# Optimization experiments

Measured on AMD Instinct MI355X. Metric: run time of the kernel, lower is better.

The kernel has to match this reference:

```python
import jax, jax.numpy as jnp
import numpy as np

B, T, V, H, E, F, NM = 128, 32, 10000, 512, 512, 2048, 512
D0 = E + NM + H   # 1536: layer-0 concat(x, h)
D1 = H + H        # 1024: layer-1 concat(h_prev_layer, h)


def setup_inputs() -> dict:
    key = jax.random.key(0)
    ks = jax.random.split(key, 10)
    cnn_features = jax.random.normal(ks[0], (B, F), jnp.float32)
    x_tokens = jax.random.randint(ks[1], (B, T), 0, V)
    current_hidden_state = jnp.zeros((2, B, 2 * H), jnp.float32)
    embedding = jax.random.normal(ks[2], (V, E), jnp.float32)
    W_in = jax.random.normal(ks[3], (F, NM), jnp.float32) / np.sqrt(F)
    b_in = jnp.zeros((NM,), jnp.float32)
    # 4 gates stacked (order: i, o, f, c) -- same math as 4 separate matmuls
    W0 = jax.random.normal(ks[4], (D0, 4 * H), jnp.float32) / np.sqrt(D0)
    b0 = jnp.full((4 * H,), 2.0, jnp.float32)
    W1 = jax.random.normal(ks[5], (D1, 4 * H), jnp.float32) / np.sqrt(D1)
    b1 = jnp.full((4 * H,), 2.0, jnp.float32)
    W_out = jax.random.normal(ks[6], (H, V), jnp.float32) / np.sqrt(H)
    b_out = jnp.zeros((V,), jnp.float32)
    return {"cnn_features": cnn_features, "x_tokens": x_tokens,
            "current_hidden_state": current_hidden_state, "embedding": embedding,
            "W_in": W_in, "b_in": b_in, "W0": W0, "b0": b0,
            "W1": W1, "b1": b1, "W_out": W_out, "b_out": b_out,
            "is_train": 1}


def _lstm_gates(z, c_prev):
    # gate order i, o, f, c matches the original cell's separate matmuls
    i_t, o_t, f_t, c_hat = jnp.split(z, 4, axis=1)
    i_t = jax.nn.sigmoid(i_t)
    o_t = jax.nn.sigmoid(o_t)
    f_t = jax.nn.sigmoid(f_t)
    c_hat = jnp.tanh(c_hat)
    c_t = f_t * c_prev + i_t * c_hat
    h_t = o_t * jnp.tanh(c_t)
    return h_t, c_t


def reference(cnn_features, x_tokens, current_hidden_state, embedding,
              W_in, b_in, W0, b0, W1, b1, W_out, b_out, is_train):
    # input_layer: Dropout (identity in eval) -> Linear -> LeakyReLU(0.01)
    proc = jax.nn.leaky_relu(cnn_features @ W_in + b_in, negative_slope=0.01)  # [B, NM]
    emb = embedding[x_tokens]  # [B, T, E] (teacher forcing: is_train=True)

    def step(hidden, emb_t):
        # layer 0: input = concat(token_emb, processed cnn features)
        x0 = jnp.concatenate([emb_t, proc], axis=1)          # [B, E+NM]
        h0, c0 = hidden[0, :, :H], hidden[0, :, H:]
        z0 = jnp.concatenate([x0, h0], axis=1) @ W0 + b0     # [B, 4H]
        h0n, c0n = _lstm_gates(z0, c0)
        # layer 1: input = h of layer 0 (already updated this timestep)
        h1, c1 = hidden[1, :, :H], hidden[1, :, H:]
        z1 = jnp.concatenate([h0n, h1], axis=1) @ W1 + b1    # [B, 4H]
        h1n, c1n = _lstm_gates(z1, c1)
        logits_t = h1n @ W_out + b_out                        # [B, V]
        new_hidden = jnp.stack([jnp.concatenate([h0n, c0n], axis=1),
                                jnp.concatenate([h1n, c1n], axis=1)], axis=0)
        return new_hidden, logits_t

    hidden, logits_seq = jax.lax.scan(step, current_hidden_state,
                                      jnp.moveaxis(emb, 1, 0))  # scan over T
    logits = jnp.moveaxis(logits_seq, 0, 1)  # [B, T, V]
    return logits, hidden
```

## Files before the change

kernel.cpp:

```cpp
#include <hip/hip_runtime.h>


typedef short s8v __attribute__((ext_vector_type(8)));
typedef float f4v __attribute__((ext_vector_type(4)));

__device__ __forceinline__ unsigned short f2bf(float f) {
  unsigned u = __float_as_uint(f);
  u += 0x7fffu + ((u >> 16) & 1u);
  return (unsigned short)(u >> 16);
}
__device__ __forceinline__ float sigm(float x) { return 1.0f / (1.0f + __expf(-x)); }
__device__ __forceinline__ float tanh_(float x) { return 1.0f - 2.0f / (1.0f + __expf(2.0f * x)); }

__device__ __forceinline__ void glds16(const unsigned short* g, unsigned short* l) {
  __builtin_amdgcn_global_load_lds((const __attribute__((address_space(1))) void*)g,
                                   (__attribute__((address_space(3))) void*)l, 16, 0, 0);
}

__global__ void k_transpose_cvt(const float* __restrict__ src, unsigned short* __restrict__ dst,
                                int R, int C) {
  __shared__ float tile[32][33];
  int c0 = blockIdx.x * 32, r0 = blockIdx.y * 32;
  int tx = threadIdx.x, ty = threadIdx.y;
#pragma unroll
  for (int i = 0; i < 4; i++) {
    int r = r0 + ty + i * 8, c = c0 + tx;
    if (r < R && c < C) tile[ty + i * 8][tx] = src[(size_t)r * C + c];
  }
  __syncthreads();
#pragma unroll
  for (int i = 0; i < 4; i++) {
    int c = c0 + ty + i * 8, r = r0 + tx;
    if (r < R && c < C) dst[(size_t)c * R + r] = f2bf(tile[tx][ty + i * 8]);
  }
}

__global__ void k_cvt_bf16(const float* __restrict__ in, unsigned short* __restrict__ out, int n4) {
  int i = blockIdx.x * 256 + threadIdx.x;
  if (i >= n4) return;
  float4 v = ((const float4*)in)[i];
  ushort4 p; p.x = f2bf(v.x); p.y = f2bf(v.y); p.z = f2bf(v.z); p.w = f2bf(v.w);
  ((ushort4*)out)[i] = p;
}

__global__ void k_gather_emb(const float* __restrict__ emb, const int* __restrict__ tok,
                             unsigned short* __restrict__ Xe) {
  int i = blockIdx.x * 256 + threadIdx.x;
  int r = i >> 7, k4 = (i & 127) * 4;
  int b = r & 127, t = r >> 7;
  int tk = tok[b * 32 + t];
  float4 v = *(const float4*)(emb + (size_t)tk * 512 + k4);
  ushort4 p; p.x = f2bf(v.x); p.y = f2bf(v.y); p.z = f2bf(v.z); p.w = f2bf(v.w);
  ((ushort4*)Xe)[i] = p;
}

__global__ void k_init_state(const float* __restrict__ chs,
                             unsigned short* __restrict__ h0b1, unsigned short* __restrict__ h1b1,
                             float* __restrict__ h0f, float* __restrict__ c0f,
                             float* __restrict__ h1f, float* __restrict__ c1f) {
  int i = blockIdx.x * 256 + threadIdx.x;
  int b = i >> 9, j = i & 511;
  float h0 = chs[b * 1024 + j], c0 = chs[b * 1024 + 512 + j];
  float h1 = chs[131072 + b * 1024 + j], c1 = chs[131072 + b * 1024 + 512 + j];
  h0f[i] = h0; c0f[i] = c0; h1f[i] = h1; c1f[i] = c1;
  h0b1[i] = f2bf(h0); h1b1[i] = f2bf(h1);
}

template <int MODE>
__global__ __launch_bounds__(256, 2)
void k_gemm(const unsigned short* __restrict__ A, const unsigned short* __restrict__ Bt,
            const float* __restrict__ bias, const float* __restrict__ add128,
            float* __restrict__ outF, unsigned short* __restrict__ outB,
            int M, int N, int K) {
  __shared__ unsigned short As[4096];
  __shared__ unsigned short Bs[4096];
  int tid = threadIdx.x;
  int wave = tid >> 6, lane = tid & 63;
  int lr = lane & 15, lq = lane >> 4;
  int wm = (wave >> 1) * 64, wn = (wave & 1) * 64;
  int m0 = blockIdx.y * 128, n0 = blockIdx.x * 128;

  f4v acc[4][4];
  f4v zero = {0.0f, 0.0f, 0.0f, 0.0f};
#pragma unroll
  for (int i = 0; i < 4; i++)
#pragma unroll
    for (int j = 0; j < 4; j++) acc[i][j] = zero;

  int srow = tid >> 2, sofs = (tid & 3) * 8;
  int ar0 = m0 + srow, ar1 = ar0 + 64;
  int br0 = n0 + srow, br1 = br0 + 64;
  if (br0 >= N) br0 = N - 1;
  if (br1 >= N) br1 = N - 1;
  const unsigned short* Ag0 = A + (size_t)ar0 * K + sofs;
  const unsigned short* Ag1 = A + (size_t)ar1 * K + sofs;
  const unsigned short* Bg0 = Bt + (size_t)br0 * K + sofs;
  const unsigned short* Bg1 = Bt + (size_t)br1 * K + sofs;
  unsigned short* lA0 = &As[tid * 8];
  unsigned short* lA1 = &As[2048 + tid * 8];
  unsigned short* lB0 = &Bs[tid * 8];
  unsigned short* lB1 = &Bs[2048 + tid * 8];

  for (int k0 = 0; k0 < K; k0 += 32) {
    glds16(Ag0 + k0, lA0);
    glds16(Ag1 + k0, lA1);
    glds16(Bg0 + k0, lB0);
    glds16(Bg1 + k0, lB1);
    __syncthreads();
    s8v af[4], bfr[4];
#pragma unroll
    for (int i = 0; i < 4; i++) af[i] = *(const s8v*)&As[(wm + i * 16 + lr) * 32 + lq * 8];
#pragma unroll
    for (int i = 0; i < 4; i++) bfr[i] = *(const s8v*)&Bs[(wn + i * 16 + lr) * 32 + lq * 8];
#pragma unroll
    for (int i = 0; i < 4; i++)
#pragma unroll
      for (int j = 0; j < 4; j++)
        acc[i][j] = __builtin_amdgcn_mfma_f32_16x16x32_bf16(af[i], bfr[j], acc[i][j], 0, 0, 0);
    __syncthreads();
  }

#pragma unroll
  for (int i = 0; i < 4; i++) {
#pragma unroll
    for (int j = 0; j < 4; j++) {
      int nn = n0 + wn + j * 16 + lr;
      if (nn >= N) continue;
#pragma unroll
      for (int r = 0; r < 4; r++) {
        int mm = m0 + wm + i * 16 + lq * 4 + r;
        float v = acc[i][j][r];
        if (MODE == 0) {
          v += bias[nn];
          v = v > 0.0f ? v : 0.01f * v;
          outB[(size_t)mm * N + nn] = f2bf(v);
        } else if (MODE == 1) {
          v += bias[nn];
          outF[(size_t)mm * N + nn] = v;
        } else if (MODE == 2) {
          v += add128[(size_t)(mm & 127) * N + nn];
          outF[(size_t)mm * N + nn] = v;
        } else {
          v += bias[nn];
          int b = mm & 127, t = mm >> 7;
          outF[(size_t)(b * 32 + t) * N + nn] = v;
        }
      }
    }
  }
}

__global__ __launch_bounds__(128)
void k_phase(const unsigned short* __restrict__ W0h_t, const unsigned short* __restrict__ W1_t,
             const float* __restrict__ Zx, const float* __restrict__ b1,
             unsigned short* __restrict__ h0b0, unsigned short* __restrict__ h0b1,
             unsigned short* __restrict__ h1b0, unsigned short* __restrict__ h1b1,
             float* __restrict__ h0f, float* __restrict__ c0f,
             float* __restrict__ h1f, float* __restrict__ c1f,
             unsigned short* __restrict__ H1all,
             int tB, int doB, int tA, int doA) {
  int wave = threadIdx.x >> 6, lane = threadIdx.x & 63;
  int gid = blockIdx.x * 2 + wave;
  bool isB = gid < 256;
  if (isB && !doB) return;
  if (!isB && !doA) return;
  int id = gid & 255;
  int mt = id >> 5, jt = id & 31;
  int lr = lane & 15, lq = lane >> 4;
  int m = mt * 16 + lr;
  f4v zero = {0.0f, 0.0f, 0.0f, 0.0f};
  f4v acc[4] = {zero, zero, zero, zero};

  if (isB) {
    const unsigned short* h0r = (tB & 1) ? h0b1 : h0b0;
    const unsigned short* h1r = (tB & 1) ? h1b0 : h1b1;
    unsigned short* h1w = (tB & 1) ? h1b1 : h1b0;
    for (int kc = 0; kc < 32; kc++) {
      int kk = kc * 32 + lq * 8;
      const unsigned short* ap = (kk < 512) ? (h0r + m * 512 + kk)
                                            : (h1r + m * 512 + kk - 512);
      s8v a = *(const s8v*)ap;
#pragma unroll
      for (int g = 0; g < 4; g++) {
        int n = g * 512 + jt * 16 + lr;
        s8v b = *(const s8v*)(W1_t + (size_t)n * 1024 + kc * 32 + lq * 8);
        acc[g] = __builtin_amdgcn_mfma_f32_16x16x32_bf16(a, b, acc[g], 0, 0, 0);
      }
    }
    int j = jt * 16 + lr;
    float bi = b1[j], bo = b1[512 + j], bff = b1[1024 + j], bc = b1[1536 + j];
#pragma unroll
    for (int r = 0; r < 4; r++) {
      int mm = mt * 16 + lq * 4 + r;
      int idx = mm * 512 + j;
      float cprev = c1f[idx];
      float iv = sigm(acc[0][r] + bi);
      float ov = sigm(acc[1][r] + bo);
      float fv = sigm(acc[2][r] + bff);
      float cv = tanh_(acc[3][r] + bc);
      float cn = fv * cprev + iv * cv;
      float hn = ov * tanh_(cn);
      c1f[idx] = cn; h1f[idx] = hn;
      unsigned short hb = f2bf(hn);
      h1w[idx] = hb;
      H1all[(size_t)(tB * 128 + mm) * 512 + j] = hb;
    }
  } else {
    const unsigned short* h0r = (tA & 1) ? h0b0 : h0b1;
    unsigned short* h0w = (tA & 1) ? h0b1 : h0b0;
    for (int kc = 0; kc < 16; kc++) {
      s8v a = *(const s8v*)(h0r + m * 512 + kc * 32 + lq * 8);
#pragma unroll
      for (int g = 0; g < 4; g++) {
        int n = g * 512 + jt * 16 + lr;
        s8v b = *(const s8v*)(W0h_t + (size_t)n * 512 + kc * 32 + lq * 8);
        acc[g] = __builtin_amdgcn_mfma_f32_16x16x32_bf16(a, b, acc[g], 0, 0, 0);
      }
    }
    int j = jt * 16 + lr;
    const float* zrow = Zx + (size_t)tA * 128 * 2048;
#pragma unroll
    for (int r = 0; r < 4; r++) {
      int mm = mt * 16 + lq * 4 + r;
      int idx = mm * 512 + j;
      float cprev = c0f[idx];
      float iv = sigm(acc[0][r] + zrow[mm * 2048 + j]);
      float ov = sigm(acc[1][r] + zrow[mm * 2048 + 512 + j]);
      float fv = sigm(acc[2][r] + zrow[mm * 2048 + 1024 + j]);
      float cv = tanh_(acc[3][r] + zrow[mm * 2048 + 1536 + j]);
      float cn = fv * cprev + iv * cv;
      float hn = ov * tanh_(cn);
      c0f[idx] = cn; h0f[idx] = hn;
      h0w[idx] = f2bf(hn);
    }
  }
}

__global__ void k_write_hidden(const float* __restrict__ h0f, const float* __restrict__ c0f,
                               const float* __restrict__ h1f, const float* __restrict__ c1f,
                               float* __restrict__ out) {
  int idx = blockIdx.x * 256 + threadIdx.x;
  int l = idx >> 17, rem = idx & 131071, b = rem >> 10, j = rem & 1023;
  const float* hs = l ? h1f : h0f;
  const float* cs = l ? c1f : c0f;
  float v = (j < 512) ? hs[b * 512 + j] : cs[b * 512 + (j - 512)];
  out[40960000 + idx] = v;
}

extern "C" void kernel_launch(void* const* d_in, const int* in_sizes, int n_in,
                              void* d_out, int out_size, void* d_ws, size_t ws_size,
                              hipStream_t stream) {
  const float* cnn  = (const float*)d_in[0];
  const int*   tok  = (const int*)d_in[1];
  const float* chs  = (const float*)d_in[2];
  const float* emb  = (const float*)d_in[3];
  const float* W_in = (const float*)d_in[4];
  const float* b_in = (const float*)d_in[5];
  const float* W0   = (const float*)d_in[6];
  const float* b0   = (const float*)d_in[7];
  const float* W1   = (const float*)d_in[8];
  const float* b1   = (const float*)d_in[9];
  const float* W_out= (const float*)d_in[10];
  const float* b_out= (const float*)d_in[11];
  float* out = (float*)d_out;

  char* p = (char*)d_ws;
  auto alloc = [&](size_t bytes) { char* q = p; p += (bytes + 255) & ~(size_t)255; return q; };
  unsigned short* Win_t  = (unsigned short*)alloc((size_t)512 * 2048 * 2);
  unsigned short* W0e_t  = (unsigned short*)alloc((size_t)2048 * 512 * 2);
  unsigned short* W0m_t  = (unsigned short*)alloc((size_t)2048 * 512 * 2);
  unsigned short* W0h_t  = (unsigned short*)alloc((size_t)2048 * 512 * 2);
  unsigned short* W1_t   = (unsigned short*)alloc((size_t)2048 * 1024 * 2);
  unsigned short* Wout_t = (unsigned short*)alloc((size_t)10000 * 512 * 2);
  unsigned short* cnn_b  = (unsigned short*)alloc((size_t)128 * 2048 * 2);
  unsigned short* proc_b = (unsigned short*)alloc((size_t)128 * 512 * 2);
  float*          Cf     = (float*)alloc((size_t)128 * 2048 * 4);
  unsigned short* Xe     = (unsigned short*)alloc((size_t)4096 * 512 * 2);
  float*          Zx     = (float*)alloc((size_t)4096 * 2048 * 4);
  unsigned short* h0b0   = (unsigned short*)alloc(65536 * 2);
  unsigned short* h0b1   = (unsigned short*)alloc(65536 * 2);
  unsigned short* h1b0   = (unsigned short*)alloc(65536 * 2);
  unsigned short* h1b1   = (unsigned short*)alloc(65536 * 2);
  float*          h0f    = (float*)alloc(65536 * 4);
  float*          c0f    = (float*)alloc(65536 * 4);
  float*          h1f    = (float*)alloc(65536 * 4);
  float*          c1f    = (float*)alloc(65536 * 4);
  unsigned short* H1all  = (unsigned short*)alloc((size_t)4096 * 512 * 2);

  dim3 tb(32, 8);
  k_transpose_cvt<<<dim3(16, 64),  tb, 0, stream>>>(W_in, Win_t, 2048, 512);
  k_transpose_cvt<<<dim3(64, 16),  tb, 0, stream>>>(W0,               W0e_t, 512, 2048);
  k_transpose_cvt<<<dim3(64, 16),  tb, 0, stream>>>(W0 + 512 * 2048,  W0m_t, 512, 2048);
  k_transpose_cvt<<<dim3(64, 16),  tb, 0, stream>>>(W0 + 1024 * 2048, W0h_t, 512, 2048);
  k_transpose_cvt<<<dim3(64, 32),  tb, 0, stream>>>(W1, W1_t, 1024, 2048);
  k_transpose_cvt<<<dim3(313, 16), tb, 0, stream>>>(W_out, Wout_t, 512, 10000);
  k_cvt_bf16<<<256, 256, 0, stream>>>(cnn, cnn_b, 65536);

  k_gemm<0><<<dim3(4, 1), 256, 0, stream>>>(cnn_b, Win_t, b_in, nullptr, nullptr, proc_b,
                                            128, 512, 2048);
  k_gemm<1><<<dim3(16, 1), 256, 0, stream>>>(proc_b, W0m_t, b0, nullptr, Cf, nullptr,
                                             128, 2048, 512);
  k_gather_emb<<<2048, 256, 0, stream>>>(emb, tok, Xe);
  k_gemm<2><<<dim3(16, 32), 256, 0, stream>>>(Xe, W0e_t, nullptr, Cf, Zx, nullptr,
                                              4096, 2048, 512);
  k_init_state<<<256, 256, 0, stream>>>(chs, h0b1, h1b1, h0f, c0f, h1f, c1f);

  k_phase<<<256, 128, 0, stream>>>(W0h_t, W1_t, Zx, b1, h0b0, h0b1, h1b0, h1b1,
                                   h0f, c0f, h1f, c1f, H1all, 0, 0, 0, 1);
  for (int t = 0; t < 32; t++)
    k_phase<<<256, 128, 0, stream>>>(W0h_t, W1_t, Zx, b1, h0b0, h0b1, h1b0, h1b1,
                                     h0f, c0f, h1f, c1f, H1all, t, 1, t + 1, (t < 31) ? 1 : 0);

  k_gemm<3><<<dim3(79, 32), 256, 0, stream>>>(H1all, Wout_t, b_out, nullptr, out, nullptr,
                                              4096, 10000, 512);
  k_write_hidden<<<1024, 256, 0, stream>>>(h0f, c0f, h1f, c1f, out);
}
```

Baseline: 873.5 us.

## Overlap per-timestep output projection with recurrent phase kernel launches

The large output-projection GEMM that ran after the recurrence is split into per-timestep slices (128x10000x512). Each slice runs in extra blocks of the next timestep's phase kernel, using the recurrent kernel's idle CUs. Phase blocks now hold 4 waves instead of 2, halving the block count to 128. The intent is to hide most of the logits GEMM behind the latency-bound recurrence. The cost is smaller, less efficient GEMM tiles and possible contention with the critical-path recurrent waves.

Measured after the change: 1.056 ms. +20.9%, slower.

```diff
diff --git a/kernel.cpp b/kernel.cpp
--- a/kernel.cpp
+++ b/kernel.cpp
@@ -137,38 +137,102 @@
         } else if (MODE == 1) {
           v += bias[nn];
           outF[(size_t)mm * N + nn] = v;
-        } else if (MODE == 2) {
+        } else {
           v += add128[(size_t)(mm & 127) * N + nn];
           outF[(size_t)mm * N + nn] = v;
-        } else {
-          v += bias[nn];
-          int b = mm & 127, t = mm >> 7;
-          outF[(size_t)(b * 32 + t) * N + nn] = v;
         }
       }
     }
   }
 }
 
-__global__ __launch_bounds__(128)
-void k_phase(const unsigned short* __restrict__ W0h_t, const unsigned short* __restrict__ W1_t,
-             const float* __restrict__ Zx, const float* __restrict__ b1,
-             unsigned short* __restrict__ h0b0, unsigned short* __restrict__ h0b1,
-             unsigned short* __restrict__ h1b0, unsigned short* __restrict__ h1b1,
-             float* __restrict__ h0f, float* __restrict__ c0f,
-             float* __restrict__ h1f, float* __restrict__ c1f,
-             unsigned short* __restrict__ H1all,
-             int tB, int doB, int tA, int doA) {
-  int wave = threadIdx.x >> 6, lane = threadIdx.x & 63;
-  int gid = blockIdx.x * 2 + wave;
+__global__ __launch_bounds__(256, 2)
+void k_phase_fused(const unsigned short* __restrict__ W0h_t, const unsigned short* __restrict__ W1_t,
+                   const float* __restrict__ Zx, const float* __restrict__ b1,
+                   unsigned short* __restrict__ h0b0, unsigned short* __restrict__ h0b1,
+                   unsigned short* __restrict__ h1b0, unsigned short* __restrict__ h1b1,
+                   float* __restrict__ h0f, float* __restrict__ c0f,
+                   float* __restrict__ h1f, float* __restrict__ c1f,
+                   unsigned short* __restrict__ H1all,
+                   const unsigned short* __restrict__ Wout_t, const float* __restrict__ b_out,
+                   float* __restrict__ out,
+                   int tB, int doB, int tA, int doA, int tL, int doL, int nPB) {
+  __shared__ unsigned short As[4096];
+  __shared__ unsigned short Bs[4096];
+  int tid = threadIdx.x;
+  int wave = tid >> 6, lane = tid & 63;
+  int lr = lane & 15, lq = lane >> 4;
+  f4v zero = {0.0f, 0.0f, 0.0f, 0.0f};
+
+  if ((int)blockIdx.x >= nPB) {
+    if (!doL) return;
+    int lb = (int)blockIdx.x - nPB;
+    int n0 = lb * 128;
+    const unsigned short* A = H1all + (size_t)tL * 128 * 512;
+    int wm = (wave >> 1) * 64, wn = (wave & 1) * 64;
+
+    f4v acc[4][4];
+#pragma unroll
+    for (int i = 0; i < 4; i++)
+#pragma unroll
+      for (int j = 0; j < 4; j++) acc[i][j] = zero;
+
+    int srow = tid >> 2, sofs = (tid & 3) * 8;
+    int ar0 = srow, ar1 = srow + 64;
+    int br0 = n0 + srow, br1 = n0 + srow + 64;
+    if (br0 > 9999) br0 = 9999;
+    if (br1 > 9999) br1 = 9999;
+    const unsigned short* Ag0 = A + (size_t)ar0 * 512 + sofs;
+    const unsigned short* Ag1 = A + (size_t)ar1 * 512 + sofs;
+    const unsigned short* Bg0 = Wout_t + (size_t)br0 * 512 + sofs;
+    const unsigned short* Bg1 = Wout_t + (size_t)br1 * 512 + sofs;
+    unsigned short* lA0 = &As[tid * 8];
+    unsigned short* lA1 = &As[2048 + tid * 8];
+    unsigned short* lB0 = &Bs[tid * 8];
+    unsigned short* lB1 = &Bs[2048 + tid * 8];
+
+    for (int k0 = 0; k0 < 512; k0 += 32) {
+      glds16(Ag0 + k0, lA0);
+      glds16(Ag1 + k0, lA1);
+      glds16(Bg0 + k0, lB0);
+      glds16(Bg1 + k0, lB1);
+      __syncthreads();
+      s8v af[4], bfr[4];
+#pragma unroll
+      for (int i = 0; i < 4; i++) af[i] = *(const s8v*)&As[(wm + i * 16 + lr) * 32 + lq * 8];
+#pragma unroll
+      for (int i = 0; i < 4; i++) bfr[i] = *(const s8v*)&Bs[(wn + i * 16 + lr) * 32 + lq * 8];
+#pragma unroll
+      for (int i = 0; i < 4; i++)
+#pragma unroll
+        for (int j = 0; j < 4; j++)
+          acc[i][j] = __builtin_amdgcn_mfma_f32_16x16x32_bf16(af[i], bfr[j], acc[i][j], 0, 0, 0);
+      __syncthreads();
+    }
+
+#pragma unroll
+    for (int i = 0; i < 4; i++) {
+#pragma unroll
+      for (int j = 0; j < 4; j++) {
+        int nn = n0 + wn + j * 16 + lr;
+        if (nn >= 10000) continue;
+#pragma unroll
+        for (int r = 0; r < 4; r++) {
+          int b = wm + i * 16 + lq * 4 + r;
+          out[(size_t)(b * 32 + tL) * 10000 + nn] = acc[i][j][r] + b_out[nn];
+        }
+      }
+    }
+    return;
+  }
+
+  int gid = (int)blockIdx.x * 4 + wave;
   bool isB = gid < 256;
   if (isB && !doB) return;
   if (!isB && !doA) return;
   int id = gid & 255;
   int mt = id >> 5, jt = id & 31;
-  int lr = lane & 15, lq = lane >> 4;
   int m = mt * 16 + lr;
-  f4v zero = {0.0f, 0.0f, 0.0f, 0.0f};
   f4v acc[4] = {zero, zero, zero, zero};
 
   if (isB) {
@@ -305,13 +369,24 @@
                                               4096, 2048, 512);
   k_init_state<<<256, 256, 0, stream>>>(chs, h0b1, h1b1, h0f, c0f, h1f, c1f);
 
-  k_phase<<<256, 128, 0, stream>>>(W0h_t, W1_t, Zx, b1, h0b0, h0b1, h1b0, h1b1,
-                                   h0f, c0f, h1f, c1f, H1all, 0, 0, 0, 1);
-  for (int t = 0; t < 32; t++)
-    k_phase<<<256, 128, 0, stream>>>(W0h_t, W1_t, Zx, b1, h0b0, h0b1, h1b0, h1b1,
-                                     h0f, c0f, h1f, c1f, H1all, t, 1, t + 1, (t < 31) ? 1 : 0);
-
-  k_gemm<3><<<dim3(79, 32), 256, 0, stream>>>(H1all, Wout_t, b_out, nullptr, out, nullptr,
-                                              4096, 10000, 512);
+  const int NPB = 128;
+  k_phase_fused<<<NPB, 256, 0, stream>>>(W0h_t, W1_t, Zx, b1, h0b0, h0b1, h1b0, h1b1,
+                                         h0f, c0f, h1f, c1f, H1all,
+                                         Wout_t, b_out, out,
+                                         0, 0, 0, 1, 0, 0, NPB);
+  for (int t = 0; t < 32; t++) {
+    int doL = (t >= 1) ? 1 : 0;
+    int grid = NPB + (doL ? 79 : 0);
+    k_phase_fused<<<grid, 256, 0, stream>>>(W0h_t, W1_t, Zx, b1, h0b0, h0b1, h1b0, h1b1,
+                                            h0f, c0f, h1f, c1f, H1all,
+                                            Wout_t, b_out, out,
+                                            t, 1, t + 1, (t < 31) ? 1 : 0,
+                                            t - 1, doL, NPB);
+  }
+  k_phase_fused<<<79, 256, 0, stream>>>(W0h_t, W1_t, Zx, b1, h0b0, h0b1, h1b0, h1b1,
+                                        h0f, c0f, h1f, c1f, H1all,
+                                        Wout_t, b_out, out,
+                                        0, 0, 0, 0, 31, 1, 0);
+
   k_write_hidden<<<1024, 256, 0, stream>>>(h0f, c0f, h1f, c1f, out);
 }
```
